# Performance work log

Measured on AMD Instinct MI355X. Metric: run time of the kernel, lower is better.

The kernel has to match this reference:

```python
import jax, jax.numpy as jnp
import numpy as np

B, S, D, U = 4, 2048, 1024, 1024

def setup_inputs() -> dict:
    key = jax.random.key(0)
    ks = jax.random.split(key, 6)
    glorot = lambda k, shape: jax.random.uniform(k, shape, jnp.float32,
                                                 -np.sqrt(6.0/(shape[0]+shape[1])),
                                                 np.sqrt(6.0/(shape[0]+shape[1])))
    return {
        "inputs": jax.random.normal(ks[0], (B, S, D), jnp.float32),
        "Wq": glorot(ks[1], (D, U)),
        "Wk": glorot(ks[2], (D, U)),
        "Wv": glorot(ks[3], (D, U)),
        "Wo": glorot(ks[4], (U, D)),
        "bo": jnp.zeros((D,), jnp.float32),
        "scale": jnp.asarray(1.0 / np.sqrt(U), jnp.float32),
    }

def reference(inputs, Wq, Wk, Wv, Wo, bo, scale):
    # q, k, v: [B, S, U]
    q = jnp.einsum('bsd,du->bsu', inputs, Wq)
    k = jnp.einsum('bsd,du->bsu', inputs, Wk)
    v = jnp.einsum('bsd,du->bsu', inputs, Wv)
    # scores: [B, S, S]
    scores = jnp.einsum('bqu,bku->bqk', q, k) * scale
    weights = jax.nn.softmax(scores, axis=-1)
    context = jnp.einsum('bqk,bku->bqu', weights, v)
    output = jnp.einsum('bsu,ud->bsd', context, Wo) + bo
    return (output, weights)
```

## Files before the change

kernel.cpp:

```cpp
#include <hip/hip_runtime.h>
#include <hip/hip_bf16.h>

#define BB 4
#define SS 2048
#define DD 1024
#define UU 1024
#define NTOK (BB*SS)

typedef __attribute__((ext_vector_type(8))) short bf16x8;
typedef __attribute__((ext_vector_type(4))) float f32x4;
typedef __attribute__((ext_vector_type(4))) unsigned short u16x4;
typedef __attribute__((ext_vector_type(8))) unsigned short u16x8;

__device__ inline unsigned short f2bf(float f) {
  unsigned u = __builtin_bit_cast(unsigned, f);
  u += 0x7FFFu + ((u >> 16) & 1u);
  return (unsigned short)(u >> 16);
}

__device__ inline void gload_lds16(const unsigned short* g, unsigned short* l) {
  __builtin_amdgcn_global_load_lds(
      (const __attribute__((address_space(1))) void*)g,
      (__attribute__((address_space(3))) void*)l, 16, 0, 0);
}

__global__ __launch_bounds__(256) void cast_f32_bf16(const float* __restrict__ in,
                                                     unsigned short* __restrict__ out,
                                                     long n) {
  long i = ((long)blockIdx.x * blockDim.x + threadIdx.x) * 4;
  long stride = (long)gridDim.x * blockDim.x * 4;
  for (long idx = i; idx < n; idx += stride) {
    float4 v = *(const float4*)(in + idx);
    u16x4 o;
    o[0] = f2bf(v.x); o[1] = f2bf(v.y); o[2] = f2bf(v.z); o[3] = f2bf(v.w);
    *(u16x4*)(out + idx) = o;
  }
}

__global__ __launch_bounds__(256) void transpose_cast_w(const float* __restrict__ in,
                                                        unsigned short* __restrict__ out,
                                                        int R, int C) {
  __shared__ float tile[32][33];
  int bx = blockIdx.x * 32;
  int by = blockIdx.y * 32;
  int tx = threadIdx.x, ty = threadIdx.y;
  #pragma unroll
  for (int j = 0; j < 32; j += 8)
    tile[ty + j][tx] = in[(long)(by + ty + j) * C + bx + tx];
  __syncthreads();
  #pragma unroll
  for (int j = 0; j < 32; j += 8)
    out[(long)(bx + ty + j) * R + by + tx] = f2bf(tile[tx][ty + j]);
}

__global__ __launch_bounds__(256) void transpose_bf16_batched(const unsigned short* __restrict__ in,
                                                              unsigned short* __restrict__ out,
                                                              int R, int C) {
  __shared__ unsigned short tile[32][34];
  long z = (long)blockIdx.z * R * C;
  int bx = blockIdx.x * 32;
  int by = blockIdx.y * 32;
  int tx = threadIdx.x, ty = threadIdx.y;
  #pragma unroll
  for (int j = 0; j < 32; j += 8)
    tile[ty + j][tx] = in[z + (long)(by + ty + j) * C + bx + tx];
  __syncthreads();
  #pragma unroll
  for (int j = 0; j < 32; j += 8)
    out[z + (long)(bx + ty + j) * R + by + tx] = tile[tx][ty + j];
}

__global__ __launch_bounds__(256) void gemm_bt_bf16(
    const unsigned short* __restrict__ A,
    const unsigned short* __restrict__ Bt,
    float* __restrict__ Cf,
    unsigned short* __restrict__ Cb,
    const float* __restrict__ bias,
    const float* __restrict__ alpha_ptr,
    int M, int N, int K,
    long sA, long sB, long sC) {
  __shared__ __align__(16) unsigned short As[128 * 64];
  __shared__ __align__(16) unsigned short Bs[128 * 64];

  const int tid = threadIdx.x;
  const int lane = tid & 63;
  const int wid = tid >> 6;
  const int wm = wid >> 1, wn = wid & 1;
  const long zA = (long)blockIdx.z * sA;
  const long zB = (long)blockIdx.z * sB;
  const long zC = (long)blockIdx.z * sC;
  const int m0 = blockIdx.y * 128;
  const int n0 = blockIdx.x * 128;

  f32x4 acc[4][4] = {};

  const int lrow = lane >> 3;
  const int lcol = (lane & 7) * 8;
  const unsigned short* Ap = A + zA + (long)(m0 + wid * 32 + lrow) * K + lcol;
  const unsigned short* Bp = Bt + zB + (long)(n0 + wid * 32 + lrow) * K + lcol;
  unsigned short* AsW = &As[(wid * 32) * 64];
  unsigned short* BsW = &Bs[(wid * 32) * 64];

  for (int k0 = 0; k0 < K; k0 += 64) {
    #pragma unroll
    for (int c = 0; c < 4; ++c) {
      gload_lds16(Ap + (long)(c * 8) * K + k0, AsW + (c * 8) * 64);
      gload_lds16(Bp + (long)(c * 8) * K + k0, BsW + (c * 8) * 64);
    }
    __syncthreads();
    #pragma unroll
    for (int kk = 0; kk < 2; ++kk) {
      bf16x8 af[4], bf_[4];
      #pragma unroll
      for (int m = 0; m < 4; ++m)
        af[m] = *(const bf16x8*)&As[(wm * 64 + m * 16 + (lane & 15)) * 64 + kk * 32 + (lane >> 4) * 8];
      #pragma unroll
      for (int n = 0; n < 4; ++n)
        bf_[n] = *(const bf16x8*)&Bs[(wn * 64 + n * 16 + (lane & 15)) * 64 + kk * 32 + (lane >> 4) * 8];
      #pragma unroll
      for (int m = 0; m < 4; ++m)
        #pragma unroll
        for (int n = 0; n < 4; ++n)
          acc[m][n] = __builtin_amdgcn_mfma_f32_16x16x32_bf16(af[m], bf_[n], acc[m][n], 0, 0, 0);
    }
    __syncthreads();
  }

  const float alpha = alpha_ptr ? *alpha_ptr : 1.0f;
  const int crow0 = m0 + wm * 64 + ((lane >> 4) * 4);
  const int ccol0 = n0 + wn * 64 + (lane & 15);
  #pragma unroll
  for (int m = 0; m < 4; ++m) {
    #pragma unroll
    for (int n = 0; n < 4; ++n) {
      const int cc = ccol0 + n * 16;
      const float bv = bias ? bias[cc] : 0.0f;
      #pragma unroll
      for (int r = 0; r < 4; ++r) {
        const int rr = crow0 + m * 16 + r;
        const float v = acc[m][n][r] * alpha + bv;
        const long idx = zC + (long)rr * N + cc;
        if (Cf) Cf[idx] = v;
        if (Cb) Cb[idx] = f2bf(v);
      }
    }
  }
}

__global__ __launch_bounds__(256) void softmax_rows(float* __restrict__ Wf,
                                                    unsigned short* __restrict__ Pb) {
  const int t = threadIdx.x;
  const int lane = t & 63, wid = t >> 6;
  const long base = (long)blockIdx.x * SS;
  float* p = Wf + base;

  float4 a = *(const float4*)(p + t * 4);
  float4 b = *(const float4*)(p + 1024 + t * 4);

  float m = fmaxf(fmaxf(fmaxf(a.x, a.y), fmaxf(a.z, a.w)),
                  fmaxf(fmaxf(b.x, b.y), fmaxf(b.z, b.w)));
  #pragma unroll
  for (int off = 32; off; off >>= 1) m = fmaxf(m, __shfl_xor(m, off));
  __shared__ float redm[4];
  __shared__ float reds[4];
  if (lane == 0) redm[wid] = m;
  __syncthreads();
  m = fmaxf(fmaxf(redm[0], redm[1]), fmaxf(redm[2], redm[3]));

  float e[8];
  e[0] = __expf(a.x - m); e[1] = __expf(a.y - m); e[2] = __expf(a.z - m); e[3] = __expf(a.w - m);
  e[4] = __expf(b.x - m); e[5] = __expf(b.y - m); e[6] = __expf(b.z - m); e[7] = __expf(b.w - m);
  float s = (e[0] + e[1]) + (e[2] + e[3]) + (e[4] + e[5]) + (e[6] + e[7]);
  #pragma unroll
  for (int off = 32; off; off >>= 1) s += __shfl_xor(s, off);
  if (lane == 0) reds[wid] = s;
  __syncthreads();
  s = (reds[0] + reds[1]) + (reds[2] + reds[3]);
  const float inv = 1.0f / s;

  float4 oa = make_float4(e[0] * inv, e[1] * inv, e[2] * inv, e[3] * inv);
  float4 ob = make_float4(e[4] * inv, e[5] * inv, e[6] * inv, e[7] * inv);
  *(float4*)(p + t * 4) = oa;
  *(float4*)(p + 1024 + t * 4) = ob;

  u16x4 ba, bb2;
  ba[0] = f2bf(oa.x); ba[1] = f2bf(oa.y); ba[2] = f2bf(oa.z); ba[3] = f2bf(oa.w);
  bb2[0] = f2bf(ob.x); bb2[1] = f2bf(ob.y); bb2[2] = f2bf(ob.z); bb2[3] = f2bf(ob.w);
  *(u16x4*)(Pb + base + t * 4) = ba;
  *(u16x4*)(Pb + base + 1024 + t * 4) = bb2;
}

extern "C" void kernel_launch(void* const* d_in, const int* in_sizes, int n_in,
                              void* d_out, int out_size, void* d_ws, size_t ws_size,
                              hipStream_t stream) {
  const float* X     = (const float*)d_in[0];
  const float* Wq    = (const float*)d_in[1];
  const float* Wk    = (const float*)d_in[2];
  const float* Wv    = (const float*)d_in[3];
  const float* Wo    = (const float*)d_in[4];
  const float* bo    = (const float*)d_in[5];
  const float* scale = (const float*)d_in[6];

  float* out = (float*)d_out;
  float* wts = out + (long)NTOK * DD;

  unsigned short* ws = (unsigned short*)d_ws;
  unsigned short* Xb  = ws;
  unsigned short* Qb  = Xb + (long)NTOK * DD;
  unsigned short* Kb  = Qb + (long)NTOK * UU;
  unsigned short* Vb  = Kb + (long)NTOK * UU;
  unsigned short* Wqt = Vb + (long)NTOK * UU;
  unsigned short* Wkt = Wqt + (long)UU * DD;
  unsigned short* Wvt = Wkt + (long)UU * DD;
  unsigned short* Wot = Wvt + (long)UU * DD;
  unsigned short* Cb  = Xb;
  unsigned short* Vt  = Qb;
  unsigned short* Pb  = Kb;

  cast_f32_bf16<<<2048, 256, 0, stream>>>(X, Xb, (long)NTOK * DD);

  transpose_cast_w<<<dim3(UU/32, DD/32), dim3(32, 8), 0, stream>>>(Wq, Wqt, DD, UU);
  transpose_cast_w<<<dim3(UU/32, DD/32), dim3(32, 8), 0, stream>>>(Wk, Wkt, DD, UU);
  transpose_cast_w<<<dim3(UU/32, DD/32), dim3(32, 8), 0, stream>>>(Wv, Wvt, DD, UU);
  transpose_cast_w<<<dim3(DD/32, UU/32), dim3(32, 8), 0, stream>>>(Wo, Wot, UU, DD);

  dim3 gProj(UU/128, NTOK/128, 1);
  gemm_bt_bf16<<<gProj, 256, 0, stream>>>(Xb, Wqt, nullptr, Qb, nullptr, nullptr,
                                          NTOK, UU, DD, 0, 0, 0);
  gemm_bt_bf16<<<gProj, 256, 0, stream>>>(Xb, Wkt, nullptr, Kb, nullptr, nullptr,
                                          NTOK, UU, DD, 0, 0, 0);
  gemm_bt_bf16<<<gProj, 256, 0, stream>>>(Xb, Wvt, nullptr, Vb, nullptr, nullptr,
                                          NTOK, UU, DD, 0, 0, 0);

  dim3 gScores(SS/128, SS/128, BB);
  gemm_bt_bf16<<<gScores, 256, 0, stream>>>(Qb, Kb, wts, nullptr, nullptr, scale,
                                            SS, SS, UU,
                                            (long)SS * UU, (long)SS * UU, (long)SS * SS);

  transpose_bf16_batched<<<dim3(UU/32, SS/32, BB), dim3(32, 8), 0, stream>>>(Vb, Vt, SS, UU);

  softmax_rows<<<BB * SS, 256, 0, stream>>>(wts, Pb);

  dim3 gPV(UU/128, SS/128, BB);
  gemm_bt_bf16<<<gPV, 256, 0, stream>>>(Pb, Vt, nullptr, Cb, nullptr, nullptr,
                                        SS, UU, SS,
                                        (long)SS * SS, (long)UU * SS, (long)SS * UU);

  dim3 gOut(DD/128, NTOK/128, 1);
  gemm_bt_bf16<<<gOut, 256, 0, stream>>>(Cb, Wot, out, nullptr, bo, nullptr,
                                         NTOK, DD, UU, 0, 0, 0);
}
```

Measured before the change: 409.7 us.

## Replace GEMM with 8-wave double-buffered ping-pong kernel using swizzled LDS

Replaces the 128x128 single-buffered GEMM with a 512-thread kernel using 256xBN tiles and double-buffered LDS. Each next k-tile's global-to-LDS loads are split across the compute phases, MFMA bursts are raised with s_setprio, and LDS columns are XOR-swizzled to avoid bank conflicts. This aims to hide global load latency behind compute and increase data reuse per block. In exchange it uses much more LDS per block, launches fewer blocks, and relies on hand-placed barriers and waitcnt that are easy to get wrong.

Result: faster. 379.6 us (-7.4%).

```diff
diff --git a/kernel.cpp b/kernel.cpp
--- a/kernel.cpp
+++ b/kernel.cpp
@@ -7,10 +7,10 @@
 #define UU 1024
 #define NTOK (BB*SS)
 
+typedef unsigned short ushort_t;
 typedef __attribute__((ext_vector_type(8))) short bf16x8;
 typedef __attribute__((ext_vector_type(4))) float f32x4;
 typedef __attribute__((ext_vector_type(4))) unsigned short u16x4;
-typedef __attribute__((ext_vector_type(8))) unsigned short u16x8;
 
 __device__ inline unsigned short f2bf(float f) {
   unsigned u = __builtin_bit_cast(unsigned, f);
@@ -18,14 +18,21 @@
   return (unsigned short)(u >> 16);
 }
 
-__device__ inline void gload_lds16(const unsigned short* g, unsigned short* l) {
+__device__ inline void gload_lds16(const ushort_t* g, ushort_t* l) {
   __builtin_amdgcn_global_load_lds(
       (const __attribute__((address_space(1))) void*)g,
       (__attribute__((address_space(3))) void*)l, 16, 0, 0);
 }
 
+#define WAIT_LGKM0 do { asm volatile("s_waitcnt lgkmcnt(0)" ::: "memory"); \
+                        __builtin_amdgcn_sched_barrier(0); } while(0)
+#define WAIT_VM0   do { asm volatile("s_waitcnt vmcnt(0)" ::: "memory"); \
+                        __builtin_amdgcn_sched_barrier(0); } while(0)
+#define BAR        do { __builtin_amdgcn_s_barrier(); \
+                        __builtin_amdgcn_sched_barrier(0); } while(0)
+
 __global__ __launch_bounds__(256) void cast_f32_bf16(const float* __restrict__ in,
-                                                     unsigned short* __restrict__ out,
+                                                     ushort_t* __restrict__ out,
                                                      long n) {
   long i = ((long)blockIdx.x * blockDim.x + threadIdx.x) * 4;
   long stride = (long)gridDim.x * blockDim.x * 4;
@@ -38,11 +45,10 @@
 }
 
 __global__ __launch_bounds__(256) void transpose_cast_w(const float* __restrict__ in,
-                                                        unsigned short* __restrict__ out,
+                                                        ushort_t* __restrict__ out,
                                                         int R, int C) {
   __shared__ float tile[32][33];
-  int bx = blockIdx.x * 32;
-  int by = blockIdx.y * 32;
+  int bx = blockIdx.x * 32, by = blockIdx.y * 32;
   int tx = threadIdx.x, ty = threadIdx.y;
   #pragma unroll
   for (int j = 0; j < 32; j += 8)
@@ -53,13 +59,12 @@
     out[(long)(bx + ty + j) * R + by + tx] = f2bf(tile[tx][ty + j]);
 }
 
-__global__ __launch_bounds__(256) void transpose_bf16_batched(const unsigned short* __restrict__ in,
-                                                              unsigned short* __restrict__ out,
+__global__ __launch_bounds__(256) void transpose_bf16_batched(const ushort_t* __restrict__ in,
+                                                              ushort_t* __restrict__ out,
                                                               int R, int C) {
-  __shared__ unsigned short tile[32][34];
+  __shared__ ushort_t tile[32][34];
   long z = (long)blockIdx.z * R * C;
-  int bx = blockIdx.x * 32;
-  int by = blockIdx.y * 32;
+  int bx = blockIdx.x * 32, by = blockIdx.y * 32;
   int tx = threadIdx.x, ty = threadIdx.y;
   #pragma unroll
   for (int j = 0; j < 32; j += 8)
@@ -70,69 +75,179 @@
     out[z + (long)(bx + ty + j) * R + by + tx] = tile[tx][ty + j];
 }
 
-__global__ __launch_bounds__(256) void gemm_bt_bf16(
-    const unsigned short* __restrict__ A,
-    const unsigned short* __restrict__ Bt,
+template<int BN>
+__global__ __launch_bounds__(512, 2) void gemm8p(
+    const ushort_t* __restrict__ A,
+    const ushort_t* __restrict__ Bt,
     float* __restrict__ Cf,
-    unsigned short* __restrict__ Cb,
+    ushort_t* __restrict__ Cb,
     const float* __restrict__ bias,
     const float* __restrict__ alpha_ptr,
     int M, int N, int K,
     long sA, long sB, long sC) {
-  __shared__ __align__(16) unsigned short As[128 * 64];
-  __shared__ __align__(16) unsigned short Bs[128 * 64];
+  static_assert(BN == 128 || BN == 256, "BN");
+  constexpr int NREP = BN / 64;
+  constexpr int BSTEPS = BN / 64;
+  __shared__ __align__(16) ushort_t As[2][256 * 64];
+  __shared__ __align__(16) ushort_t Bs[2][BN * 64];
 
   const int tid = threadIdx.x;
   const int lane = tid & 63;
   const int wid = tid >> 6;
-  const int wm = wid >> 1, wn = wid & 1;
+  const int wm = wid >> 2, wn = wid & 3;
   const long zA = (long)blockIdx.z * sA;
   const long zB = (long)blockIdx.z * sB;
   const long zC = (long)blockIdx.z * sC;
-  const int m0 = blockIdx.y * 128;
-  const int n0 = blockIdx.x * 128;
-
-  f32x4 acc[4][4] = {};
-
-  const int lrow = lane >> 3;
-  const int lcol = (lane & 7) * 8;
-  const unsigned short* Ap = A + zA + (long)(m0 + wid * 32 + lrow) * K + lcol;
-  const unsigned short* Bp = Bt + zB + (long)(n0 + wid * 32 + lrow) * K + lcol;
-  unsigned short* AsW = &As[(wid * 32) * 64];
-  unsigned short* BsW = &Bs[(wid * 32) * 64];
-
-  for (int k0 = 0; k0 < K; k0 += 64) {
+  const int m0 = blockIdx.y * 256;
+  const int n0 = blockIdx.x * BN;
+
+  f32x4 acc[8][NREP] = {};
+
+  const int srow = tid >> 3;
+  const int cs = (tid & 7) ^ (srow & 7);
+  const ushort_t* Aps = A + zA + (long)(m0 + srow) * K + cs * 8;
+  const ushort_t* Bps = Bt + zB + (long)(n0 + srow) * K + cs * 8;
+  const int ldst = (wid * 64) * 8;
+
+  const int rsel = (lane & 15);
+  const int csel = (lane >> 4);
+  const int cxor = (lane & 7);
+
+  const int nt = K / 64;
+
+  #pragma unroll
+  for (int j = 0; j < 4; ++j)
+    gload_lds16(Aps + (long)(j * 64) * K, &As[0][j * 4096 + ldst]);
+  #pragma unroll
+  for (int j = 0; j < BSTEPS; ++j)
+    gload_lds16(Bps + (long)(j * 64) * K, &Bs[0][j * 4096 + ldst]);
+  WAIT_VM0;
+  BAR;
+
+  for (int t = 0; t < nt; ++t) {
+    const int cur = t & 1, nxt = cur ^ 1;
+    const int k1 = (t + 1) * 64;
+    const bool pf = (t + 1 < nt);
+    const ushort_t* __restrict__ Ac = &As[cur][0];
+    const ushort_t* __restrict__ Bc = &Bs[cur][0];
+
+    bf16x8 bfr[NREP][2], af[4][2];
+
     #pragma unroll
-    for (int c = 0; c < 4; ++c) {
-      gload_lds16(Ap + (long)(c * 8) * K + k0, AsW + (c * 8) * 64);
-      gload_lds16(Bp + (long)(c * 8) * K + k0, BsW + (c * 8) * 64);
+    for (int n = 0; n < NREP; ++n)
+      #pragma unroll
+      for (int kk = 0; kk < 2; ++kk)
+        bfr[n][kk] = *(const bf16x8*)&Bc[(wn * (BN/4) + n * 16 + rsel) * 64
+                                         + ((kk * 4 + csel) ^ cxor) * 8];
+    #pragma unroll
+    for (int m = 0; m < 4; ++m)
+      #pragma unroll
+      for (int kk = 0; kk < 2; ++kk)
+        af[m][kk] = *(const bf16x8*)&Ac[(wm * 128 + m * 16 + rsel) * 64
+                                        + ((kk * 4 + csel) ^ cxor) * 8];
+    if (pf) {
+      gload_lds16(Aps + (long)(0 * 64) * K + k1, &As[nxt][0 * 4096 + ldst]);
+      gload_lds16(Aps + (long)(1 * 64) * K + k1, &As[nxt][1 * 4096 + ldst]);
+      gload_lds16(Bps + (long)(0 * 64) * K + k1, &Bs[nxt][0 * 4096 + ldst]);
+      if (BN == 256)
+        gload_lds16(Bps + (long)(1 * 64) * K + k1, &Bs[nxt][1 * 4096 + ldst]);
     }
-    __syncthreads();
+    BAR;
+    WAIT_LGKM0;
+    __builtin_amdgcn_s_setprio(1);
     #pragma unroll
-    for (int kk = 0; kk < 2; ++kk) {
-      bf16x8 af[4], bf_[4];
-      #pragma unroll
-      for (int m = 0; m < 4; ++m)
-        af[m] = *(const bf16x8*)&As[(wm * 64 + m * 16 + (lane & 15)) * 64 + kk * 32 + (lane >> 4) * 8];
-      #pragma unroll
-      for (int n = 0; n < 4; ++n)
-        bf_[n] = *(const bf16x8*)&Bs[(wn * 64 + n * 16 + (lane & 15)) * 64 + kk * 32 + (lane >> 4) * 8];
-      #pragma unroll
-      for (int m = 0; m < 4; ++m)
-        #pragma unroll
-        for (int n = 0; n < 4; ++n)
-          acc[m][n] = __builtin_amdgcn_mfma_f32_16x16x32_bf16(af[m], bf_[n], acc[m][n], 0, 0, 0);
+    for (int m = 0; m < 4; ++m)
+      #pragma unroll
+      for (int n = 0; n < (NREP == 4 ? 2 : NREP); ++n)
+        #pragma unroll
+        for (int kk = 0; kk < 2; ++kk)
+          acc[m][n] = __builtin_amdgcn_mfma_f32_16x16x32_bf16(af[m][kk], bfr[n][kk], acc[m][n], 0, 0, 0);
+    __builtin_amdgcn_s_setprio(0);
+    BAR;
+
+    if (NREP == 4) {
+      if (pf) {
+        gload_lds16(Aps + (long)(2 * 64) * K + k1, &As[nxt][2 * 4096 + ldst]);
+        gload_lds16(Aps + (long)(3 * 64) * K + k1, &As[nxt][3 * 4096 + ldst]);
+        gload_lds16(Bps + (long)(2 * 64) * K + k1, &Bs[nxt][2 * 4096 + ldst]);
+        gload_lds16(Bps + (long)(3 * 64) * K + k1, &Bs[nxt][3 * 4096 + ldst]);
+      }
+      BAR;
+      __builtin_amdgcn_s_setprio(1);
+      #pragma unroll
+      for (int m = 0; m < 4; ++m)
+        #pragma unroll
+        for (int n = 2; n < 4; ++n)
+          #pragma unroll
+          for (int kk = 0; kk < 2; ++kk)
+            acc[m][n] = __builtin_amdgcn_mfma_f32_16x16x32_bf16(af[m][kk], bfr[n][kk], acc[m][n], 0, 0, 0);
+      __builtin_amdgcn_s_setprio(0);
+      BAR;
+
+      #pragma unroll
+      for (int m = 0; m < 4; ++m)
+        #pragma unroll
+        for (int kk = 0; kk < 2; ++kk)
+          af[m][kk] = *(const bf16x8*)&Ac[(wm * 128 + 64 + m * 16 + rsel) * 64
+                                          + ((kk * 4 + csel) ^ cxor) * 8];
+      BAR;
+      WAIT_LGKM0;
+      __builtin_amdgcn_s_setprio(1);
+      #pragma unroll
+      for (int m = 0; m < 4; ++m)
+        #pragma unroll
+        for (int n = 0; n < 2; ++n)
+          #pragma unroll
+          for (int kk = 0; kk < 2; ++kk)
+            acc[m + 4][n] = __builtin_amdgcn_mfma_f32_16x16x32_bf16(af[m][kk], bfr[n][kk], acc[m + 4][n], 0, 0, 0);
+      __builtin_amdgcn_s_setprio(0);
+      BAR;
+
+      __builtin_amdgcn_s_setprio(1);
+      #pragma unroll
+      for (int m = 0; m < 4; ++m)
+        #pragma unroll
+        for (int n = 2; n < 4; ++n)
+          #pragma unroll
+          for (int kk = 0; kk < 2; ++kk)
+            acc[m + 4][n] = __builtin_amdgcn_mfma_f32_16x16x32_bf16(af[m][kk], bfr[n][kk], acc[m + 4][n], 0, 0, 0);
+      __builtin_amdgcn_s_setprio(0);
+    } else {
+      #pragma unroll
+      for (int m = 0; m < 4; ++m)
+        #pragma unroll
+        for (int kk = 0; kk < 2; ++kk)
+          af[m][kk] = *(const bf16x8*)&Ac[(wm * 128 + 64 + m * 16 + rsel) * 64
+                                          + ((kk * 4 + csel) ^ cxor) * 8];
+      if (pf) {
+        gload_lds16(Aps + (long)(2 * 64) * K + k1, &As[nxt][2 * 4096 + ldst]);
+        gload_lds16(Aps + (long)(3 * 64) * K + k1, &As[nxt][3 * 4096 + ldst]);
+        gload_lds16(Bps + (long)(1 * 64) * K + k1, &Bs[nxt][1 * 4096 + ldst]);
+      }
+      BAR;
+      WAIT_LGKM0;
+      __builtin_amdgcn_s_setprio(1);
+      #pragma unroll
+      for (int m = 0; m < 4; ++m)
+        #pragma unroll
+        for (int n = 0; n < NREP; ++n)
+          #pragma unroll
+          for (int kk = 0; kk < 2; ++kk)
+            acc[m + 4][n] = __builtin_amdgcn_mfma_f32_16x16x32_bf16(af[m][kk], bfr[n][kk], acc[m + 4][n], 0, 0, 0);
+      __builtin_amdgcn_s_setprio(0);
     }
-    __syncthreads();
+
+    WAIT_VM0;
+    BAR;
   }
 
   const float alpha = alpha_ptr ? *alpha_ptr : 1.0f;
-  const int crow0 = m0 + wm * 64 + ((lane >> 4) * 4);
-  const int ccol0 = n0 + wn * 64 + (lane & 15);
-  #pragma unroll
-  for (int m = 0; m < 4; ++m) {
+  const int crow0 = m0 + wm * 128 + csel * 4;
+  const int ccol0 = n0 + wn * (BN / 4) + rsel;
+  #pragma unroll
+  for (int m = 0; m < 8; ++m) {
     #pragma unroll
-    for (int n = 0; n < 4; ++n) {
+    for (int n = 0; n < NREP; ++n) {
       const int cc = ccol0 + n * 16;
       const float bv = bias ? bias[cc] : 0.0f;
       #pragma unroll
@@ -148,7 +263,7 @@
 }
 
 __global__ __launch_bounds__(256) void softmax_rows(float* __restrict__ Wf,
-                                                    unsigned short* __restrict__ Pb) {
+                                                    ushort_t* __restrict__ Pb) {
   const int t = threadIdx.x;
   const int lane = t & 63, wid = t >> 6;
   const long base = (long)blockIdx.x * SS;
@@ -204,18 +319,18 @@
   float* out = (float*)d_out;
   float* wts = out + (long)NTOK * DD;
 
-  unsigned short* ws = (unsigned short*)d_ws;
-  unsigned short* Xb  = ws;
-  unsigned short* Qb  = Xb + (long)NTOK * DD;
-  unsigned short* Kb  = Qb + (long)NTOK * UU;
-  unsigned short* Vb  = Kb + (long)NTOK * UU;
-  unsigned short* Wqt = Vb + (long)NTOK * UU;
-  unsigned short* Wkt = Wqt + (long)UU * DD;
-  unsigned short* Wvt = Wkt + (long)UU * DD;
-  unsigned short* Wot = Wvt + (long)UU * DD;
-  unsigned short* Cb  = Xb;
-  unsigned short* Vt  = Qb;
-  unsigned short* Pb  = Kb;
+  ushort_t* ws = (ushort_t*)d_ws;
+  ushort_t* Xb  = ws;
+  ushort_t* Qb  = Xb + (long)NTOK * DD;
+  ushort_t* Kb  = Qb + (long)NTOK * UU;
+  ushort_t* Vb  = Kb + (long)NTOK * UU;
+  ushort_t* Wqt = Vb + (long)NTOK * UU;
+  ushort_t* Wkt = Wqt + (long)UU * DD;
+  ushort_t* Wvt = Wkt + (long)UU * DD;
+  ushort_t* Wot = Wvt + (long)UU * DD;
+  ushort_t* Cb  = Xb;
+  ushort_t* Vt  = Qb;
+  ushort_t* Pb  = Kb;
 
   cast_f32_bf16<<<2048, 256, 0, stream>>>(X, Xb, (long)NTOK * DD);
 
@@ -224,29 +339,29 @@
   transpose_cast_w<<<dim3(UU/32, DD/32), dim3(32, 8), 0, stream>>>(Wv, Wvt, DD, UU);
   transpose_cast_w<<<dim3(DD/32, UU/32), dim3(32, 8), 0, stream>>>(Wo, Wot, UU, DD);
 
-  dim3 gProj(UU/128, NTOK/128, 1);
-  gemm_bt_bf16<<<gProj, 256, 0, stream>>>(Xb, Wqt, nullptr, Qb, nullptr, nullptr,
-                                          NTOK, UU, DD, 0, 0, 0);
-  gemm_bt_bf16<<<gProj, 256, 0, stream>>>(Xb, Wkt, nullptr, Kb, nullptr, nullptr,
-                                          NTOK, UU, DD, 0, 0, 0);
-  gemm_bt_bf16<<<gProj, 256, 0, stream>>>(Xb, Wvt, nullptr, Vb, nullptr, nullptr,
-                                          NTOK, UU, DD, 0, 0, 0);
-
-  dim3 gScores(SS/128, SS/128, BB);
-  gemm_bt_bf16<<<gScores, 256, 0, stream>>>(Qb, Kb, wts, nullptr, nullptr, scale,
-                                            SS, SS, UU,
-                                            (long)SS * UU, (long)SS * UU, (long)SS * SS);
+  dim3 gProj(UU/128, NTOK/256, 1);
+  gemm8p<128><<<gProj, 512, 0, stream>>>(Xb, Wqt, nullptr, Qb, nullptr, nullptr,
+                                         NTOK, UU, DD, 0, 0, 0);
+  gemm8p<128><<<gProj, 512, 0, stream>>>(Xb, Wkt, nullptr, Kb, nullptr, nullptr,
+                                         NTOK, UU, DD, 0, 0, 0);
+  gemm8p<128><<<gProj, 512, 0, stream>>>(Xb, Wvt, nullptr, Vb, nullptr, nullptr,
+                                         NTOK, UU, DD, 0, 0, 0);
+
+  dim3 gScores(SS/256, SS/256, BB);
+  gemm8p<256><<<gScores, 512, 0, stream>>>(Qb, Kb, wts, nullptr, nullptr, scale,
+                                           SS, SS, UU,
+                                           (long)SS * UU, (long)SS * UU, (long)SS * SS);
 
   transpose_bf16_batched<<<dim3(UU/32, SS/32, BB), dim3(32, 8), 0, stream>>>(Vb, Vt, SS, UU);
 
   softmax_rows<<<BB * SS, 256, 0, stream>>>(wts, Pb);
 
-  dim3 gPV(UU/128, SS/128, BB);
-  gemm_bt_bf16<<<gPV, 256, 0, stream>>>(Pb, Vt, nullptr, Cb, nullptr, nullptr,
-                                        SS, UU, SS,
-                                        (long)SS * SS, (long)UU * SS, (long)SS * UU);
-
-  dim3 gOut(DD/128, NTOK/128, 1);
-  gemm_bt_bf16<<<gOut, 256, 0, stream>>>(Cb, Wot, out, nullptr, bo, nullptr,
-                                         NTOK, DD, UU, 0, 0, 0);
-}
+  dim3 gPV(UU/128, SS/256, BB);
+  gemm8p<128><<<gPV, 512, 0, stream>>>(Pb, Vt, nullptr, Cb, nullptr, nullptr,
+                                       SS, UU, SS,
+                                       (long)SS * SS, (long)UU * SS, (long)SS * UU);
+
+  dim3 gOut(DD/128, NTOK/256, 1);
+  gemm8p<128><<<gOut, 512, 0, stream>>>(Cb, Wot, out, nullptr, bo, nullptr,
+                                        NTOK, DD, UU, 0, 0, 0);
+}
```
